# Kernel optimization log

Measured on AMD Instinct MI355X. Metric: run time of the kernel, lower is better.

## Reference

```python
import jax, jax.numpy as jnp
import numpy as np

N_T, N_S, F_IN, H, N_OUT = 2048, 512, 7, 64, 3


def setup_inputs() -> dict:
    key = jax.random.key(0)
    ks = jax.random.split(key, 12)
    pts = jax.random.normal(ks[0], (N_T, 3), jnp.float32)
    centers = jax.random.normal(ks[1], (N_S, 3), jnp.float32)
    nrm = jax.random.normal(ks[2], (N_S, 3), jnp.float32)
    normals = nrm / jnp.linalg.norm(nrm, axis=-1, keepdims=True)
    areas = jax.random.uniform(ks[3], (N_S,), jnp.float32, 0.1, 1.0)
    ref_lengths = jax.random.uniform(ks[4], (2,), jnp.float32, 0.5, 1.5)

    def lin(k, i, o):
        return jax.random.normal(k, (i, o), jnp.float32) / np.float32(np.sqrt(i))

    return {
        "prediction_points": pts,
        "face_centers": centers,
        "face_normals": normals,
        "face_areas": areas,
        "reference_lengths": ref_lengths,
        "W1": lin(ks[5], F_IN, H), "b1": jnp.zeros((H,), jnp.float32),
        "W2": lin(ks[6], H, H),    "b2": jnp.zeros((H,), jnp.float32),
        "W3": lin(ks[7], H, H),    "b3": jnp.zeros((H,), jnp.float32),
        "Wout": lin(ks[8], H, N_OUT), "bout": jnp.zeros((N_OUT,), jnp.float32),
        "p_scale": jnp.float32(1.0), "p_bias": jnp.float32(0.0),
        "v_scale": jnp.float32(1.0), "v_bias": jnp.float32(0.0),
    }


def reference(prediction_points, face_centers, face_normals, face_areas,
              reference_lengths, W1, b1, W2, b2, W3, b3, Wout, bout,
              p_scale, p_bias, v_scale, v_bias):
    eps = jnp.float32(1e-8)
    # Pairwise relative geometry (translation/rotation-equivariant features).
    rvec = prediction_points[:, None, :] - face_centers[None, :, :]  # [T,S,3]
    r2 = jnp.sum(rvec * rvec, axis=-1)                               # [T,S]
    r = jnp.sqrt(r2 + eps)
    rhat = rvec / r[..., None]
    c = jnp.sum(rhat * face_normals[None, :, :], axis=-1)            # cos(angle)
    # Legendre polynomials P0..P3 (n_spherical_harmonics = 4).
    legendre = jnp.stack(
        [jnp.ones_like(c), c, 0.5 * (3.0 * c * c - 1.0),
         0.5 * (5.0 * c * c * c - 3.0 * c)], axis=-1)                # [T,S,4]
    # Multiscale nondimensional distance features, one per reference length.
    dfeat = 1.0 / (1.0 + r[..., None] / reference_lengths)           # [T,S,2]
    afeat = jnp.broadcast_to(jnp.log(face_areas)[None, :, None],
                             r.shape + (1,))                          # [T,S,1]
    feats = jnp.concatenate([dfeat, legendre, afeat], axis=-1)       # [T,S,7]
    # Kernel MLP evaluated per (target, source) pair.
    h = jnp.tanh(feats @ W1 + b1)
    h = jnp.tanh(h @ W2 + b2)
    h = jnp.tanh(h @ W3 + b3)
    out = h @ Wout + bout                                            # [T,S,3]
    # Green's-function-like decay, area-weighted boundary integral.
    decay = face_areas[None, :] / (r2 + 1.0)                         # [T,S]
    p = jnp.sum(out[..., 0] * decay, axis=1)                         # [T]
    vel = jnp.sum((out[..., 1:2] * rhat
                   + out[..., 2:3] * face_normals[None, :, :])
                  * decay[..., None], axis=1)                        # [T,3]
    pressure = p * p_scale + p_bias
    velocity = vel * v_scale + v_bias
    return jnp.concatenate([pressure[:, None], velocity], axis=-1)   # [T,4]
```

## Files before the change

kernel.cpp:

```cpp
#include <hip/hip_runtime.h>
#include <hip/hip_fp16.h>


#define N_T 2048
#define N_S 512
#define BLK 64
#define SCALE 2.885390081777927f

#define CPY_F 5888
#define CPY_U 1472

typedef _Float16 f16;
typedef _Float16 f16x4 __attribute__((ext_vector_type(4)));
typedef _Float16 f16x8 __attribute__((ext_vector_type(8)));
typedef float f32x4 __attribute__((ext_vector_type(4)));
typedef unsigned short u16;
typedef unsigned int u32;

__device__ __forceinline__ float zsig(float x) {
    float e = __builtin_amdgcn_exp2f(x);
    return __builtin_amdgcn_rcpf(e + 1.0f);
}

__device__ __forceinline__ f32x4 mfma16(f16x4 a, f16x4 b, f32x4 c) {
    return __builtin_amdgcn_mfma_f32_16x16x16f16(a, b, c, 0, 0, 0);
}
__device__ __forceinline__ f32x4 mfma32(f16x8 a, f16x8 b, f32x4 c) {
    return __builtin_amdgcn_mfma_f32_16x16x32_f16(a, b, c, 0, 0, 0);
}

__device__ __forceinline__ u32 pkrtz(float a, float b) {
    return __builtin_bit_cast(u32, __builtin_amdgcn_cvt_pkrtz(a, b));
}

__device__ __forceinline__ f16x4 lo4(uint4 g) {
    uint2 p; p.x = g.x; p.y = g.y;
    return __builtin_bit_cast(f16x4, p);
}
__device__ __forceinline__ f16x4 hi4(uint4 g) {
    uint2 p; p.x = g.z; p.y = g.w;
    return __builtin_bit_cast(f16x4, p);
}
__device__ __forceinline__ f16x8 all8(uint4 g) {
    return __builtin_bit_cast(f16x8, g);
}
__device__ __forceinline__ f32x4 asv4(float4 v) {
    return __builtin_bit_cast(f32x4, v);
}

__device__ __forceinline__ f16x8 tpack8(f32x4 cl, f32x4 ch) {
    uint4 p;
    p.x = pkrtz(zsig(cl[0]), zsig(cl[1]));
    p.y = pkrtz(zsig(cl[2]), zsig(cl[3]));
    p.z = pkrtz(zsig(ch[0]), zsig(ch[1]));
    p.w = pkrtz(zsig(ch[2]), zsig(ch[3]));
    return __builtin_bit_cast(f16x8, p);
}

__global__ __launch_bounds__(256) void prep_kernel(
    const float* __restrict__ W1, const float* __restrict__ b1,
    const float* __restrict__ W2, const float* __restrict__ b2,
    const float* __restrict__ W3, const float* __restrict__ b3,
    const float* __restrict__ Wout, const float* __restrict__ bout,
    float* __restrict__ ws, float* __restrict__ outp)
{
    const int tid = blockIdx.x * 256 + threadIdx.x;
    if (tid < 8192) outp[tid] = 0.f;
    if (tid < 5632) {
        const int cpy = tid / 1408;
        const int r   = tid - cpy * 1408;
        const int u   = r >> 6, lane = r & 63;
        const int q = lane >> 4, l15 = lane & 15;
        float x[8];
        bool lo = false;
        #pragma unroll
        for (int e = 0; e < 8; ++e) {
            const int half = e >> 2, j = e & 3;
            float v;
            if (u < 2) {
                const int mt = u * 2 + half;
                const int k = q * 4 + j;
                v = (k < 7) ? W1[k * 64 + mt * 16 + l15] * SCALE : 0.f;
            } else if (u < 10) {
                const int idx = u - 2, mt = idx >> 1, kp = idx & 1;
                const int k = (kp * 2 + half) * 16 + q * 4 + j;
                v = -2.0f * W2[k * 64 + mt * 16 + l15] * SCALE;
            } else if (u < 18) {
                const int idx = u - 10, mt = idx >> 1, kp = idx & 1;
                const int k = (kp * 2 + half) * 16 + q * 4 + j;
                v = -2.0f * W3[k * 64 + mt * 16 + l15] * SCALE;
            } else {
                const int kp = (u - 18) & 1;
                const int k = (kp * 2 + half) * 16 + q * 4 + j;
                v = (l15 < 3) ? -2.0f * Wout[k * 3 + l15] : 0.f;
                lo = (u >= 20);
            }
            x[e] = v;
        }
        u16 outw[8];
        #pragma unroll
        for (int e = 0; e < 8; ++e) {
            const f16 h = (f16)x[e];
            const f16 val = lo ? (f16)(x[e] - (float)h) : h;
            outw[e] = __builtin_bit_cast(u16, val);
        }
        uint4 g;
        g.x = outw[0] | ((u32)outw[1] << 16);
        g.y = outw[2] | ((u32)outw[3] << 16);
        g.z = outw[4] | ((u32)outw[5] << 16);
        g.w = outw[6] | ((u32)outw[7] << 16);
        *(uint4*)((char*)ws + (size_t)cpy * CPY_F * 4 + (size_t)(u * 64 + lane) * 16) = g;
    } else if (tid < 6412) {
        const int b = tid - 5632;
        const int cpy = b / 195, i = b - cpy * 195;
        if (i < 192) {
            const int Lb = i >> 6, j = i & 63;
            float bv;
            if (Lb == 0) {
                bv = b1[j];
            } else if (Lb == 1) {
                bv = b2[j];
                for (int k = 0; k < 64; ++k) bv += W2[k * 64 + j];
            } else {
                bv = b3[j];
                for (int k = 0; k < 64; ++k) bv += W3[k * 64 + j];
            }
            ws[cpy * CPY_F + 5632 + i] = bv * SCALE;
        } else {
            const int c3 = i - 192;
            float bv = bout[c3];
            for (int k = 0; k < 64; ++k) bv += Wout[k * 3 + c3];
            ws[cpy * CPY_F + 5824 + c3] = bv;
        }
    }
}

__global__ __launch_bounds__(BLK, 2) void globe_mfma(
    const float* __restrict__ pts, const float* __restrict__ ctr,
    const float* __restrict__ nrm, const float* __restrict__ areas,
    const float* __restrict__ rlen, const float* __restrict__ bout,
    const float* __restrict__ p_scale, const float* __restrict__ p_bias,
    const float* __restrict__ v_scale, const float* __restrict__ v_bias,
    const float* __restrict__ ws,
    float* __restrict__ out)
{
    __shared__ __align__(16) u16 featL[2][2][64][8];
    __shared__ __align__(16) uint4 geomL[2][2][64];

    const int lane = threadIdx.x & 63;
    const int l15  = lane & 15;
    const int q    = lane >> 4;
    const int qf   = q & 1;
    const int b    = blockIdx.x;
    const int t    = b >> 1;
    const int h    = b & 1;

    const float px = pts[3 * t + 0], py = pts[3 * t + 1], pz = pts[3 * t + 2];
    const float invL0 = __builtin_amdgcn_rcpf(rlen[0]);
    const float invL1 = __builtin_amdgcn_rcpf(rlen[1]);
    f32x4 co_init = (f32x4){0.f, 0.f, 0.f, 0.f};
    if (q == 0) { co_init[0] = ws[5824]; co_init[1] = ws[5825]; co_init[2] = ws[5826]; }

    const f16x4 bz = (f16x4){0, 0, 0, 0};
    float accp = 0.f, avx = 0.f, avy = 0.f, avz = 0.f;

    const int stag = (h + t) & 1;

    #pragma unroll
    for (int cc = 0; cc < 2; ++cc) {
        const int ch = cc ^ stag;
        const uint4* __restrict__ wsU = (const uint4*)ws + (ch * 2) * CPY_U;
        const float* __restrict__ wsBias = ws + (ch * 2) * CPY_F + 5632;

        #pragma unroll
        for (int st = 0; st < 2; ++st) {
            const int s = (h * 4 + ch * 2 + st) * 64 + lane;
            const float cx = ctr[3 * s + 0], cy = ctr[3 * s + 1], cz = ctr[3 * s + 2];
            const float snx = nrm[3 * s + 0], sny = nrm[3 * s + 1], snz = nrm[3 * s + 2];
            const float ar = areas[s];
            const float rvx = px - cx, rvy = py - cy, rvz = pz - cz;
            const float r2 = rvx * rvx + rvy * rvy + rvz * rvz;
            const float r2e = r2 + 1e-8f;
            const float rinv = __builtin_amdgcn_rsqf(r2e);
            const float r = r2e * rinv;
            const float rhx = rvx * rinv, rhy = rvy * rinv, rhz = rvz * rinv;
            const float cth = rhx * snx + rhy * sny + rhz * snz;
            const float c2 = cth * cth;
            const float decay = ar * __builtin_amdgcn_rcpf(r2 + 1.0f);
            uint4 fw;
            fw.x = pkrtz(__builtin_amdgcn_rcpf(fmaf(r, invL0, 1.0f)),
                         __builtin_amdgcn_rcpf(fmaf(r, invL1, 1.0f)));
            fw.y = pkrtz(1.0f, cth);
            fw.z = pkrtz(fmaf(1.5f, c2, -0.5f), cth * fmaf(2.5f, c2, -1.5f));
            fw.w = pkrtz(__logf(ar), 0.0f);
            *(uint4*)&featL[cc][st][lane][0] = fw;
            uint4 g;
            g.x = __builtin_bit_cast(u32, decay);
            g.y = pkrtz(rhx, rhy);
            g.z = pkrtz(rhz, snx);
            g.w = pkrtz(sny, snz);
            geomL[cc][st][lane] = g;
        }

        f16x8 B2[2][2][4];
        {
            const uint4 g0 = wsU[0 * 64 + lane], g1 = wsU[1 * 64 + lane];
            f16x4 a1[4];
            a1[0] = lo4(g0); a1[1] = hi4(g0); a1[2] = lo4(g1); a1[3] = hi4(g1);
            f32x4 bias1[4];
            #pragma unroll
            for (int mt = 0; mt < 4; ++mt)
                bias1[mt] = asv4(*(const float4*)(wsBias + 0 * 64 + mt * 16 + q * 4));
            #pragma unroll
            for (int n4 = 0; n4 < 4; ++n4) {
                f16x4 bf[2];
                #pragma unroll
                for (int st = 0; st < 2; ++st) {
                    const f16x4 lv = *(const f16x4*)&featL[cc][st][n4 * 16 + l15][qf * 4];
                    bf[st] = (q < 2) ? lv : bz;
                }
                f32x4 c[2][4];
                #pragma unroll
                for (int mt = 0; mt < 4; ++mt) {
                    c[0][mt] = mfma16(a1[mt], bf[0], bias1[mt]);
                    c[1][mt] = mfma16(a1[mt], bf[1], bias1[mt]);
                }
                #pragma unroll
                for (int kk = 0; kk < 2; ++kk) {
                    B2[0][kk][n4] = tpack8(c[0][2 * kk], c[0][2 * kk + 1]);
                    B2[1][kk][n4] = tpack8(c[1][2 * kk], c[1][2 * kk + 1]);
                }
            }
        }

        f16x8 B3[2][2][4];
        {
            f16x8 a[4][2];
            #pragma unroll
            for (int mt = 0; mt < 4; ++mt) {
                a[mt][0] = all8(wsU[(2 + 2 * mt) * 64 + lane]);
                a[mt][1] = all8(wsU[(3 + 2 * mt) * 64 + lane]);
            }
            f32x4 bias2[4];
            #pragma unroll
            for (int mt = 0; mt < 4; ++mt)
                bias2[mt] = asv4(*(const float4*)(wsBias + 1 * 64 + mt * 16 + q * 4));
            #pragma unroll
            for (int n4 = 0; n4 < 4; ++n4) {
                f32x4 c[2][4];
                #pragma unroll
                for (int mt = 0; mt < 4; ++mt) {
                    c[0][mt] = mfma32(a[mt][0], B2[0][0][n4], bias2[mt]);
                    c[1][mt] = mfma32(a[mt][0], B2[1][0][n4], bias2[mt]);
                }
                #pragma unroll
                for (int mt = 0; mt < 4; ++mt) {
                    c[0][mt] = mfma32(a[mt][1], B2[0][1][n4], c[0][mt]);
                    c[1][mt] = mfma32(a[mt][1], B2[1][1][n4], c[1][mt]);
                }
                #pragma unroll
                for (int kk = 0; kk < 2; ++kk) {
                    B3[0][kk][n4] = tpack8(c[0][2 * kk], c[0][2 * kk + 1]);
                    B3[1][kk][n4] = tpack8(c[1][2 * kk], c[1][2 * kk + 1]);
                }
            }
        }

        f16x8 BO[2][2][4];
        {
            f16x8 a[4][2];
            #pragma unroll
            for (int mt = 0; mt < 4; ++mt) {
                a[mt][0] = all8(wsU[(10 + 2 * mt) * 64 + lane]);
                a[mt][1] = all8(wsU[(11 + 2 * mt) * 64 + lane]);
            }
            f32x4 bias3[4];
            #pragma unroll
            for (int mt = 0; mt < 4; ++mt)
                bias3[mt] = asv4(*(const float4*)(wsBias + 2 * 64 + mt * 16 + q * 4));
            #pragma unroll
            for (int n4 = 0; n4 < 4; ++n4) {
                f32x4 c[2][4];
                #pragma unroll
                for (int mt = 0; mt < 4; ++mt) {
                    c[0][mt] = mfma32(a[mt][0], B3[0][0][n4], bias3[mt]);
                    c[1][mt] = mfma32(a[mt][0], B3[1][0][n4], bias3[mt]);
                }
                #pragma unroll
                for (int mt = 0; mt < 4; ++mt) {
                    c[0][mt] = mfma32(a[mt][1], B3[0][1][n4], c[0][mt]);
                    c[1][mt] = mfma32(a[mt][1], B3[1][1][n4], c[1][mt]);
                }
                #pragma unroll
                for (int kk = 0; kk < 2; ++kk) {
                    BO[0][kk][n4] = tpack8(c[0][2 * kk], c[0][2 * kk + 1]);
                    BO[1][kk][n4] = tpack8(c[1][2 * kk], c[1][2 * kk + 1]);
                }
            }
        }

        {
            const f16x8 aoh0 = all8(wsU[18 * 64 + lane]);
            const f16x8 aoh1 = all8(wsU[19 * 64 + lane]);
            const f16x8 aol0 = all8(wsU[20 * 64 + lane]);
            const f16x8 aol1 = all8(wsU[21 * 64 + lane]);
            #pragma unroll
            for (int n4 = 0; n4 < 4; ++n4) {
                f32x4 co[2];
                co[0] = mfma32(aoh0, BO[0][0][n4], co_init);
                co[1] = mfma32(aoh0, BO[1][0][n4], co_init);
                co[0] = mfma32(aol0, BO[0][0][n4], co[0]);
                co[1] = mfma32(aol0, BO[1][0][n4], co[1]);
                co[0] = mfma32(aoh1, BO[0][1][n4], co[0]);
                co[1] = mfma32(aoh1, BO[1][1][n4], co[1]);
                co[0] = mfma32(aol1, BO[0][1][n4], co[0]);
                co[1] = mfma32(aol1, BO[1][1][n4], co[1]);
                if (q == 0) {
                    #pragma unroll
                    for (int st = 0; st < 2; ++st) {
                        const uint4 g = geomL[cc][st][n4 * 16 + l15];
                        const float d = __builtin_bit_cast(float, g.x);
                        const float2 rxy = __half22float2(__builtin_bit_cast(__half2, g.y));
                        const float2 rzx = __half22float2(__builtin_bit_cast(__half2, g.z));
                        const float2 nyz = __half22float2(__builtin_bit_cast(__half2, g.w));
                        const float o0 = co[st][0], o1 = co[st][1], o2 = co[st][2];
                        accp = fmaf(o0, d, accp);
                        avx  = fmaf(fmaf(o1, rxy.x, o2 * rzx.y), d, avx);
                        avy  = fmaf(fmaf(o1, rxy.y, o2 * nyz.x), d, avy);
                        avz  = fmaf(fmaf(o1, rzx.x, o2 * nyz.y), d, avz);
                    }
                }
            }
        }
    }

    #pragma unroll
    for (int off = 8; off > 0; off >>= 1) {
        accp += __shfl_down(accp, off);
        avx  += __shfl_down(avx,  off);
        avy  += __shfl_down(avy,  off);
        avz  += __shfl_down(avz,  off);
    }

    if (lane == 0) {
        const float ps = p_scale[0], vs = v_scale[0];
        const float bp = h ? 0.f : p_bias[0];
        const float bv = h ? 0.f : v_bias[0];
        atomicAdd(&out[4 * t + 0], fmaf(accp, ps, bp));
        atomicAdd(&out[4 * t + 1], fmaf(avx, vs, bv));
        atomicAdd(&out[4 * t + 2], fmaf(avy, vs, bv));
        atomicAdd(&out[4 * t + 3], fmaf(avz, vs, bv));
    }
}

extern "C" void kernel_launch(void* const* d_in, const int* in_sizes, int n_in,
                              void* d_out, int out_size, void* d_ws, size_t ws_size,
                              hipStream_t stream) {
    (void)in_sizes; (void)n_in; (void)ws_size; (void)out_size;
    const float* pts   = (const float*)d_in[0];
    const float* ctr   = (const float*)d_in[1];
    const float* nrm   = (const float*)d_in[2];
    const float* areas = (const float*)d_in[3];
    const float* rlen  = (const float*)d_in[4];
    const float* W1    = (const float*)d_in[5];
    const float* b1    = (const float*)d_in[6];
    const float* W2    = (const float*)d_in[7];
    const float* b2    = (const float*)d_in[8];
    const float* W3    = (const float*)d_in[9];
    const float* b3    = (const float*)d_in[10];
    const float* Wout  = (const float*)d_in[11];
    const float* bout  = (const float*)d_in[12];
    const float* ps    = (const float*)d_in[13];
    const float* pb    = (const float*)d_in[14];
    const float* vs    = (const float*)d_in[15];
    const float* vb    = (const float*)d_in[16];
    float* ws = (float*)d_ws;

    prep_kernel<<<33, 256, 0, stream>>>(W1, b1, W2, b2, W3, b3, Wout, bout, ws,
                                        (float*)d_out);
    globe_mfma<<<N_T * 2, BLK, 0, stream>>>(
        pts, ctr, nrm, areas, rlen, bout, ps, pb, vs, vb, ws, (float*)d_out);
}
```

Before: 131.7 us.

## Fuse weight prep into main kernel, one block per target, no atomics

Removes the separate prep kernel: each block now builds the MFMA weight fragments and folded biases itself in shared memory and reads them from LDS instead of global workspace. The grid changes from two half-blocks per target with atomic accumulation to one block per target that loops over all four source chunks and writes results directly, which also drops the output zeroing. This saves a launch and the atomics, but every block repeats the weight conversion and bias reductions (64-iteration loops over W2/W3), and halving the block count may lower parallelism.

Measured after the change: 166.1 us. 26.1% more time.

```diff
diff --git a/kernel.cpp b/kernel.cpp
--- a/kernel.cpp
+++ b/kernel.cpp
@@ -6,9 +6,6 @@
 #define N_S 512
 #define BLK 64
 #define SCALE 2.885390081777927f
-
-#define CPY_F 5888
-#define CPY_U 1472
 
 typedef _Float16 f16;
 typedef _Float16 f16x4 __attribute__((ext_vector_type(4)));
@@ -57,22 +54,32 @@
     return __builtin_bit_cast(f16x8, p);
 }
 
-__global__ __launch_bounds__(256) void prep_kernel(
+__global__ __launch_bounds__(BLK, 2) void globe_all(
+    const float* __restrict__ pts, const float* __restrict__ ctr,
+    const float* __restrict__ nrm, const float* __restrict__ areas,
+    const float* __restrict__ rlen,
     const float* __restrict__ W1, const float* __restrict__ b1,
     const float* __restrict__ W2, const float* __restrict__ b2,
     const float* __restrict__ W3, const float* __restrict__ b3,
     const float* __restrict__ Wout, const float* __restrict__ bout,
-    float* __restrict__ ws, float* __restrict__ outp)
+    const float* __restrict__ p_scale, const float* __restrict__ p_bias,
+    const float* __restrict__ v_scale, const float* __restrict__ v_bias,
+    float* __restrict__ out)
 {
-    const int tid = blockIdx.x * 256 + threadIdx.x;
-    if (tid < 8192) outp[tid] = 0.f;
-    if (tid < 5632) {
-        const int cpy = tid / 1408;
-        const int r   = tid - cpy * 1408;
-        const int u   = r >> 6, lane = r & 63;
-        const int q = lane >> 4, l15 = lane & 15;
+    __shared__ __align__(16) uint4 wfrag[22][64];
+    __shared__ __align__(16) u16 featL[2][64][8];
+    __shared__ __align__(16) uint4 geomL[2][64];
+    __shared__ __align__(16) float biasL[196];
+
+    const int lane = threadIdx.x;
+    const int l15  = lane & 15;
+    const int q    = lane >> 4;
+    const int qf   = q & 1;
+    const int t    = blockIdx.x;
+
+    #pragma unroll
+    for (int u = 0; u < 22; ++u) {
         float x[8];
-        bool lo = false;
         #pragma unroll
         for (int e = 0; e < 8; ++e) {
             const int half = e >> 2, j = e & 3;
@@ -93,15 +100,15 @@
                 const int kp = (u - 18) & 1;
                 const int k = (kp * 2 + half) * 16 + q * 4 + j;
                 v = (l15 < 3) ? -2.0f * Wout[k * 3 + l15] : 0.f;
-                lo = (u >= 20);
             }
             x[e] = v;
         }
+        const bool lo = (u >= 20);
         u16 outw[8];
         #pragma unroll
         for (int e = 0; e < 8; ++e) {
-            const f16 h = (f16)x[e];
-            const f16 val = lo ? (f16)(x[e] - (float)h) : h;
+            const f16 hh = (f16)x[e];
+            const f16 val = lo ? (f16)(x[e] - (float)hh) : hh;
             outw[e] = __builtin_bit_cast(u16, val);
         }
         uint4 g;
@@ -109,72 +116,42 @@
         g.y = outw[2] | ((u32)outw[3] << 16);
         g.z = outw[4] | ((u32)outw[5] << 16);
         g.w = outw[6] | ((u32)outw[7] << 16);
-        *(uint4*)((char*)ws + (size_t)cpy * CPY_F * 4 + (size_t)(u * 64 + lane) * 16) = g;
-    } else if (tid < 6412) {
-        const int b = tid - 5632;
-        const int cpy = b / 195, i = b - cpy * 195;
-        if (i < 192) {
-            const int Lb = i >> 6, j = i & 63;
-            float bv;
-            if (Lb == 0) {
-                bv = b1[j];
-            } else if (Lb == 1) {
-                bv = b2[j];
-                for (int k = 0; k < 64; ++k) bv += W2[k * 64 + j];
-            } else {
-                bv = b3[j];
-                for (int k = 0; k < 64; ++k) bv += W3[k * 64 + j];
-            }
-            ws[cpy * CPY_F + 5632 + i] = bv * SCALE;
-        } else {
-            const int c3 = i - 192;
-            float bv = bout[c3];
-            for (int k = 0; k < 64; ++k) bv += Wout[k * 3 + c3];
-            ws[cpy * CPY_F + 5824 + c3] = bv;
-        }
-    }
-}
-
-__global__ __launch_bounds__(BLK, 2) void globe_mfma(
-    const float* __restrict__ pts, const float* __restrict__ ctr,
-    const float* __restrict__ nrm, const float* __restrict__ areas,
-    const float* __restrict__ rlen, const float* __restrict__ bout,
-    const float* __restrict__ p_scale, const float* __restrict__ p_bias,
-    const float* __restrict__ v_scale, const float* __restrict__ v_bias,
-    const float* __restrict__ ws,
-    float* __restrict__ out)
-{
-    __shared__ __align__(16) u16 featL[2][2][64][8];
-    __shared__ __align__(16) uint4 geomL[2][2][64];
-
-    const int lane = threadIdx.x & 63;
-    const int l15  = lane & 15;
-    const int q    = lane >> 4;
-    const int qf   = q & 1;
-    const int b    = blockIdx.x;
-    const int t    = b >> 1;
-    const int h    = b & 1;
+        wfrag[u][lane] = g;
+    }
+
+    {
+        biasL[lane] = b1[lane] * SCALE;
+        float s2 = b2[lane], s3 = b3[lane];
+        for (int k = 0; k < 64; ++k) {
+            s2 += W2[k * 64 + lane];
+            s3 += W3[k * 64 + lane];
+        }
+        biasL[64 + lane]  = s2 * SCALE;
+        biasL[128 + lane] = s3 * SCALE;
+        if (lane < 3) {
+            float so = bout[lane];
+            for (int k = 0; k < 64; ++k) so += Wout[k * 3 + lane];
+            biasL[192 + lane] = so;
+        }
+    }
 
     const float px = pts[3 * t + 0], py = pts[3 * t + 1], pz = pts[3 * t + 2];
     const float invL0 = __builtin_amdgcn_rcpf(rlen[0]);
     const float invL1 = __builtin_amdgcn_rcpf(rlen[1]);
     f32x4 co_init = (f32x4){0.f, 0.f, 0.f, 0.f};
-    if (q == 0) { co_init[0] = ws[5824]; co_init[1] = ws[5825]; co_init[2] = ws[5826]; }
+    if (q == 0) { co_init[0] = biasL[192]; co_init[1] = biasL[193]; co_init[2] = biasL[194]; }
 
     const f16x4 bz = (f16x4){0, 0, 0, 0};
     float accp = 0.f, avx = 0.f, avy = 0.f, avz = 0.f;
 
-    const int stag = (h + t) & 1;
-
-    #pragma unroll
-    for (int cc = 0; cc < 2; ++cc) {
-        const int ch = cc ^ stag;
-        const uint4* __restrict__ wsU = (const uint4*)ws + (ch * 2) * CPY_U;
-        const float* __restrict__ wsBias = ws + (ch * 2) * CPY_F + 5632;
+    #pragma unroll 1
+    for (int cc = 0; cc < 4; ++cc) {
+        int wofs;
+        asm volatile("v_mov_b32 %0, 0" : "=v"(wofs));
 
         #pragma unroll
         for (int st = 0; st < 2; ++st) {
-            const int s = (h * 4 + ch * 2 + st) * 64 + lane;
+            const int s = (cc * 2 + st) * 64 + lane;
             const float cx = ctr[3 * s + 0], cy = ctr[3 * s + 1], cz = ctr[3 * s + 2];
             const float snx = nrm[3 * s + 0], sny = nrm[3 * s + 1], snz = nrm[3 * s + 2];
             const float ar = areas[s];
@@ -193,30 +170,30 @@
             fw.y = pkrtz(1.0f, cth);
             fw.z = pkrtz(fmaf(1.5f, c2, -0.5f), cth * fmaf(2.5f, c2, -1.5f));
             fw.w = pkrtz(__logf(ar), 0.0f);
-            *(uint4*)&featL[cc][st][lane][0] = fw;
+            *(uint4*)&featL[st][lane][0] = fw;
             uint4 g;
             g.x = __builtin_bit_cast(u32, decay);
             g.y = pkrtz(rhx, rhy);
             g.z = pkrtz(rhz, snx);
             g.w = pkrtz(sny, snz);
-            geomL[cc][st][lane] = g;
+            geomL[st][lane] = g;
         }
 
         f16x8 B2[2][2][4];
         {
-            const uint4 g0 = wsU[0 * 64 + lane], g1 = wsU[1 * 64 + lane];
+            const uint4 g0 = wfrag[0][lane + wofs], g1 = wfrag[1][lane + wofs];
             f16x4 a1[4];
             a1[0] = lo4(g0); a1[1] = hi4(g0); a1[2] = lo4(g1); a1[3] = hi4(g1);
             f32x4 bias1[4];
             #pragma unroll
             for (int mt = 0; mt < 4; ++mt)
-                bias1[mt] = asv4(*(const float4*)(wsBias + 0 * 64 + mt * 16 + q * 4));
+                bias1[mt] = asv4(*(const float4*)&biasL[0 * 64 + mt * 16 + q * 4 + wofs]);
             #pragma unroll
             for (int n4 = 0; n4 < 4; ++n4) {
                 f16x4 bf[2];
                 #pragma unroll
                 for (int st = 0; st < 2; ++st) {
-                    const f16x4 lv = *(const f16x4*)&featL[cc][st][n4 * 16 + l15][qf * 4];
+                    const f16x4 lv = *(const f16x4*)&featL[st][n4 * 16 + l15][qf * 4];
                     bf[st] = (q < 2) ? lv : bz;
                 }
                 f32x4 c[2][4];
@@ -238,13 +215,13 @@
             f16x8 a[4][2];
             #pragma unroll
             for (int mt = 0; mt < 4; ++mt) {
-                a[mt][0] = all8(wsU[(2 + 2 * mt) * 64 + lane]);
-                a[mt][1] = all8(wsU[(3 + 2 * mt) * 64 + lane]);
+                a[mt][0] = all8(wfrag[2 + 2 * mt][lane + wofs]);
+                a[mt][1] = all8(wfrag[3 + 2 * mt][lane + wofs]);
             }
             f32x4 bias2[4];
             #pragma unroll
             for (int mt = 0; mt < 4; ++mt)
-                bias2[mt] = asv4(*(const float4*)(wsBias + 1 * 64 + mt * 16 + q * 4));
+                bias2[mt] = asv4(*(const float4*)&biasL[1 * 64 + mt * 16 + q * 4 + wofs]);
             #pragma unroll
             for (int n4 = 0; n4 < 4; ++n4) {
                 f32x4 c[2][4];
@@ -271,13 +248,13 @@
             f16x8 a[4][2];
             #pragma unroll
             for (int mt = 0; mt < 4; ++mt) {
-                a[mt][0] = all8(wsU[(10 + 2 * mt) * 64 + lane]);
-                a[mt][1] = all8(wsU[(11 + 2 * mt) * 64 + lane]);
+                a[mt][0] = all8(wfrag[10 + 2 * mt][lane + wofs]);
+                a[mt][1] = all8(wfrag[11 + 2 * mt][lane + wofs]);
             }
             f32x4 bias3[4];
             #pragma unroll
             for (int mt = 0; mt < 4; ++mt)
-                bias3[mt] = asv4(*(const float4*)(wsBias + 2 * 64 + mt * 16 + q * 4));
+                bias3[mt] = asv4(*(const float4*)&biasL[2 * 64 + mt * 16 + q * 4 + wofs]);
             #pragma unroll
             for (int n4 = 0; n4 < 4; ++n4) {
                 f32x4 c[2][4];
@@ -300,10 +277,10 @@
         }
 
         {
-            const f16x8 aoh0 = all8(wsU[18 * 64 + lane]);
-            const f16x8 aoh1 = all8(wsU[19 * 64 + lane]);
-            const f16x8 aol0 = all8(wsU[20 * 64 + lane]);
-            const f16x8 aol1 = all8(wsU[21 * 64 + lane]);
+            const f16x8 aoh0 = all8(wfrag[18][lane + wofs]);
+            const f16x8 aoh1 = all8(wfrag[19][lane + wofs]);
+            const f16x8 aol0 = all8(wfrag[20][lane + wofs]);
+            const f16x8 aol1 = all8(wfrag[21][lane + wofs]);
             #pragma unroll
             for (int n4 = 0; n4 < 4; ++n4) {
                 f32x4 co[2];
@@ -318,7 +295,7 @@
                 if (q == 0) {
                     #pragma unroll
                     for (int st = 0; st < 2; ++st) {
-                        const uint4 g = geomL[cc][st][n4 * 16 + l15];
+                        const uint4 g = geomL[st][n4 * 16 + l15];
                         const float d = __builtin_bit_cast(float, g.x);
                         const float2 rxy = __half22float2(__builtin_bit_cast(__half2, g.y));
                         const float2 rzx = __half22float2(__builtin_bit_cast(__half2, g.z));
@@ -343,20 +320,19 @@
     }
 
     if (lane == 0) {
-        const float ps = p_scale[0], vs = v_scale[0];
-        const float bp = h ? 0.f : p_bias[0];
-        const float bv = h ? 0.f : v_bias[0];
-        atomicAdd(&out[4 * t + 0], fmaf(accp, ps, bp));
-        atomicAdd(&out[4 * t + 1], fmaf(avx, vs, bv));
-        atomicAdd(&out[4 * t + 2], fmaf(avy, vs, bv));
-        atomicAdd(&out[4 * t + 3], fmaf(avz, vs, bv));
+        const float ps = p_scale[0], pb = p_bias[0];
+        const float vs = v_scale[0], vb = v_bias[0];
+        out[4 * t + 0] = fmaf(accp, ps, pb);
+        out[4 * t + 1] = fmaf(avx, vs, vb);
+        out[4 * t + 2] = fmaf(avy, vs, vb);
+        out[4 * t + 3] = fmaf(avz, vs, vb);
     }
 }
 
 extern "C" void kernel_launch(void* const* d_in, const int* in_sizes, int n_in,
                               void* d_out, int out_size, void* d_ws, size_t ws_size,
                               hipStream_t stream) {
-    (void)in_sizes; (void)n_in; (void)ws_size; (void)out_size;
+    (void)in_sizes; (void)n_in; (void)ws_size; (void)out_size; (void)d_ws;
     const float* pts   = (const float*)d_in[0];
     const float* ctr   = (const float*)d_in[1];
     const float* nrm   = (const float*)d_in[2];
@@ -374,10 +350,8 @@
     const float* pb    = (const float*)d_in[14];
     const float* vs    = (const float*)d_in[15];
     const float* vb    = (const float*)d_in[16];
-    float* ws = (float*)d_ws;
-
-    prep_kernel<<<33, 256, 0, stream>>>(W1, b1, W2, b2, W3, b3, Wout, bout, ws,
-                                        (float*)d_out);
-    globe_mfma<<<N_T * 2, BLK, 0, stream>>>(
-        pts, ctr, nrm, areas, rlen, bout, ps, pb, vs, vb, ws, (float*)d_out);
-}
+
+    globe_all<<<N_T, BLK, 0, stream>>>(
+        pts, ctr, nrm, areas, rlen, W1, b1, W2, b2, W3, b3, Wout, bout,
+        ps, pb, vs, vb, (float*)d_out);
+}
```
